# Kernel tuning notes

Hardware: AMD Instinct MI355X
Metric: run time of the kernel (lower is better)

The kernel has to match this reference:

```python
import jax, jax.numpy as jnp
import numpy as np

N_USERS = 50000
N_ITEMS = 50000
E = 400000
S = 128   # in_feats_s (memory / GRU hidden)
T = 64    # in_feats_t (time encoding dim)
ED = 64   # edge feature dim
M = 2 * S + T + ED  # in_feats_m = 384

_BASIS_FREQ = jnp.asarray(1.0 / 10 ** np.linspace(0, 9, T), dtype=jnp.float32)


def time_encode(ts):
    # cos(ts * freq + phase), phase == 0
    return jnp.cos(ts[:, None] * _BASIS_FREQ[None, :])


def mean_message(src_mem, dst_mem, ts, e, src, dst, n_dst):
    # mail per edge: [E, 2S + T + ED]
    mail = jnp.concatenate(
        [src_mem[src], dst_mem[dst], time_encode(ts), e], axis=1)
    s = jax.ops.segment_sum(mail, dst, num_segments=n_dst)
    cnt = jax.ops.segment_sum(jnp.ones_like(ts), dst, num_segments=n_dst)
    return s / jnp.maximum(cnt, 1.0)[:, None]


def gru_step(x, h, w_ih, w_hh, b_ih, b_hh):
    # single-step PyTorch GRU; gate order r, z, n
    gi = x @ w_ih.T + b_ih
    gh = h @ w_hh.T + b_hh
    ir, iz, i_n = jnp.split(gi, 3, axis=1)
    hr, hz, h_n = jnp.split(gh, 3, axis=1)
    r = jax.nn.sigmoid(ir + hr)
    z = jax.nn.sigmoid(iz + hz)
    n = jnp.tanh(i_n + r * h_n)
    return (1.0 - z) * n + z * h


def setup_inputs() -> dict:
    key = jax.random.key(0)
    ks = jax.random.split(key, 16)
    sc = 1.0 / np.sqrt(S)
    return {
        "si":   jax.random.normal(ks[0], (N_USERS, S), jnp.float32),
        "sj":   jax.random.normal(ks[1], (N_ITEMS, S), jnp.float32),
        "si_r": jax.random.normal(ks[2], (N_ITEMS, S), jnp.float32),
        "sj_r": jax.random.normal(ks[3], (N_USERS, S), jnp.float32),
        "t":    jax.random.uniform(ks[4], (E,), jnp.float32),
        "t_r":  jax.random.uniform(ks[5], (E,), jnp.float32),
        "e":    jax.random.normal(ks[6], (E, ED), jnp.float32),
        "e_r":  jax.random.normal(ks[7], (E, ED), jnp.float32),
        "w_ih": jax.random.normal(ks[8], (3 * S, M), jnp.float32) * sc,
        "w_hh": jax.random.normal(ks[9], (3 * S, S), jnp.float32) * sc,
        "b_ih": jax.random.normal(ks[10], (3 * S,), jnp.float32) * sc,
        "b_hh": jax.random.normal(ks[11], (3 * S,), jnp.float32) * sc,
        "src_g":  jax.random.randint(ks[12], (E,), 0, N_USERS, jnp.int32),
        "dst_g":  jax.random.randint(ks[13], (E,), 0, N_ITEMS, jnp.int32),
        "src_gr": jax.random.randint(ks[14], (E,), 0, N_ITEMS, jnp.int32),
        "dst_gr": jax.random.randint(ks[15], (E,), 0, N_USERS, jnp.int32),
    }


def reference(si, sj, si_r, sj_r, t, t_r, e, e_r,
              w_ih, w_hh, b_ih, b_hh,
              src_g, dst_g, src_gr, dst_gr):
    # g: user -> item; g_r: item -> user
    mj = mean_message(si, sj, t, e, src_g, dst_g, N_ITEMS)       # messages to items
    mi = mean_message(si_r, sj_r, t_r, e_r, src_gr, dst_gr, N_USERS)  # messages to users
    si_out = gru_step(mi, sj_r, w_ih, w_hh, b_ih, b_hh)  # user memory update
    sj_out = gru_step(mj, sj, w_ih, w_hh, b_ih, b_hh)    # item memory update
    return (si_out, sj_out)
```

## Files before the change

### kernel.cpp

```cpp
#include <hip/hip_runtime.h>
#include <math.h>

#define NUSERS 50000
#define NITEMS 50000
#define NTOT   100000
#define NNODE  50000
#define NCHUNK 196
#define MTILES 6250
#define KDIM   512
#define NWAVES 8192

typedef __attribute__((ext_vector_type(4))) float f32x4;
typedef __attribute__((ext_vector_type(8))) short short8;
typedef unsigned int u32;

#define AS1 __attribute__((address_space(1)))
#define AS3 __attribute__((address_space(3)))

static __device__ __forceinline__ unsigned short f2bf(float f) {
  unsigned int u = __float_as_uint(f);
  u += 0x7fffu + ((u >> 16) & 1u);
  return (unsigned short)(u >> 16);
}

static __device__ __forceinline__ u32 pack2(float x, float y) {
  return (u32)f2bf(x) | ((u32)f2bf(y) << 16);
}

static __device__ __forceinline__ void gload_lds16(const void* g, void* l) {
  __builtin_amdgcn_global_load_lds((const AS1 u32*)g, (AS3 u32*)l, 16, 0, 0);
}

__global__ void pack_w_kernel(const float* __restrict__ w_ih,
                              const float* __restrict__ w_hh,
                              const float* __restrict__ b_ih,
                              const float* __restrict__ b_hh,
                              unsigned short* __restrict__ Wb,
                              float* __restrict__ bb) {
  int idx = blockIdx.x * 256 + threadIdx.x;
  int j = idx & 7, l = (idx >> 3) & 63, ktt = idx >> 9;
  int kt = ktt & 15, tt = ktt >> 4;
  int g = tt * 16 + (l & 15);
  int k = kt * 32 + (l >> 4) * 8 + j;
  float v;
  if (g < 256)      v = (k < 384) ? w_ih[g * 384 + k] : w_hh[g * 128 + (k - 384)];
  else if (g < 384) v = (k < 384) ? w_ih[g * 384 + k] : 0.0f;
  else              v = (k < 384) ? 0.0f : w_hh[(g - 128) * 128 + (k - 384)];
  Wb[idx] = f2bf(v);
  if (idx < 512) {
    float b = (idx < 256) ? (b_ih[idx] + b_hh[idx])
            : (idx < 384) ? b_ih[idx]
                          : b_hh[idx - 128];
    bb[idx] = b;
  }
}

__global__ void cast_mem_kernel(const float* __restrict__ si,
                                const float* __restrict__ si_r,
                                unsigned short* __restrict__ si_b,
                                unsigned short* __restrict__ sir_b) {
  int i = blockIdx.x * 256 + threadIdx.x;
  const float* src; unsigned short* dst; int off;
  if (i < 800000) { src = si;   dst = si_b;  off = i; }
  else            { src = si_r; dst = sir_b; off = i - 800000; }
  const f32x4* p = (const f32x4*)(src + (size_t)off * 8);
  f32x4 a = p[0], b = p[1];
  short8 o;
  o[0] = f2bf(a[0]); o[1] = f2bf(a[1]); o[2] = f2bf(a[2]); o[3] = f2bf(a[3]);
  o[4] = f2bf(b[0]); o[5] = f2bf(b[1]); o[6] = f2bf(b[2]); o[7] = f2bf(b[3]);
  *(short8*)(dst + (size_t)off * 8) = o;
}

__global__ void hist_kernel(const int* __restrict__ dst_g,
                            const int* __restrict__ dst_gr,
                            int* __restrict__ deg_j, int* __restrict__ deg_i, int E) {
  int i = blockIdx.x * 256 + threadIdx.x;
  if (i < E) atomicAdd(&deg_j[dst_g[i]], 1);
  else if (i < 2 * E) atomicAdd(&deg_i[dst_gr[i - E]], 1);
}

__global__ void chunksum_kernel(const int* __restrict__ deg_j,
                                const int* __restrict__ deg_i,
                                int* __restrict__ csum) {
  int c = blockIdx.x;
  const int* deg = (c < NCHUNK) ? deg_j : deg_i;
  int cc = (c < NCHUNK) ? c : c - NCHUNK;
  int t = threadIdx.x;
  int idx = cc * 256 + t;
  int v = (idx < NNODE) ? deg[idx] : 0;
  for (int off = 32; off; off >>= 1) v += __shfl_down(v, off, 64);
  __shared__ int wsum[4];
  if ((t & 63) == 0) wsum[t >> 6] = v;
  __syncthreads();
  if (t == 0) csum[c] = wsum[0] + wsum[1] + wsum[2] + wsum[3];
}

__global__ void chunkscan_kernel(const int* __restrict__ csum, int* __restrict__ coff) {
  int d = blockIdx.x;
  const int* cs = csum + d * NCHUNK;
  int* co = coff + d * NCHUNK;
  int t = threadIdx.x, lane = t & 63, w = t >> 6;
  int v = (t < NCHUNK) ? cs[t] : 0;
  int x = v;
  for (int off = 1; off < 64; off <<= 1) {
    int y = __shfl_up(x, off, 64);
    if (lane >= off) x += y;
  }
  __shared__ int wt[4];
  if (lane == 63) wt[w] = x;
  __syncthreads();
  int add = 0;
  for (int k = 0; k < 4; ++k) if (k < w) add += wt[k];
  if (t < NCHUNK) co[t] = add + x - v;
}

__global__ void localscan_kernel(const int* __restrict__ deg_j,
                                 const int* __restrict__ deg_i,
                                 const int* __restrict__ coff,
                                 int* __restrict__ rs_j, int* __restrict__ cur_j,
                                 int* __restrict__ rs_i, int* __restrict__ cur_i) {
  int c = blockIdx.x;
  bool dj = c < NCHUNK;
  const int* deg = dj ? deg_j : deg_i;
  int cc = dj ? c : c - NCHUNK;
  int* rs = dj ? rs_j : rs_i;
  int* cur = dj ? cur_j : cur_i;
  int base = coff[c];
  int t = threadIdx.x, lane = t & 63, w = t >> 6;
  int idx = cc * 256 + t;
  int v = (idx < NNODE) ? deg[idx] : 0;
  int x = v;
  for (int off = 1; off < 64; off <<= 1) {
    int y = __shfl_up(x, off, 64);
    if (lane >= off) x += y;
  }
  __shared__ int wt[4];
  if (lane == 63) wt[w] = x;
  __syncthreads();
  int add = 0;
  for (int k = 0; k < 4; ++k) if (k < w) add += wt[k];
  int ex = base + add + x - v;
  if (idx < NNODE) { rs[idx] = ex; cur[idx] = ex; }
}

__global__ void fill_kernel(const int* __restrict__ src_g, const int* __restrict__ dst_g,
                            const float* __restrict__ t,
                            const int* __restrict__ src_gr, const int* __restrict__ dst_gr,
                            const float* __restrict__ t_r,
                            int* __restrict__ cur_j, int* __restrict__ cur_i,
                            int4* __restrict__ recP_j, int4* __restrict__ recP_i,
                            int E) {
  int i = blockIdx.x * 256 + threadIdx.x;
  if (i < E) {
    int pos = atomicAdd(&cur_j[dst_g[i]], 1);
    recP_j[pos] = make_int4(src_g[i], i, __float_as_int(t[i]), 0);
  } else if (i < 2 * E) {
    int k = i - E;
    int pos = atomicAdd(&cur_i[dst_gr[k]], 1);
    recP_i[pos] = make_int4(src_gr[k], k, __float_as_int(t_r[k]), 0);
  }
}

__global__ __launch_bounds__(256) void gather_kernel(
    const unsigned short* __restrict__ si_b, const unsigned short* __restrict__ sir_b,
    const float* __restrict__ sj, const float* __restrict__ sj_r,
    const float* __restrict__ e, const float* __restrict__ e_r,
    const int* __restrict__ rs_j, const int* __restrict__ rs_i,
    const int* __restrict__ deg_j, const int* __restrict__ deg_i,
    const int4* __restrict__ recP_j, const int4* __restrict__ recP_i,
    unsigned short* __restrict__ Xb) {
  __shared__ __align__(16) unsigned short rowbuf[4][512];
  int wid = threadIdx.x >> 6, lane = threadIdx.x & 63;
  int gwave = blockIdx.x * 4 + wid;
  float freq = __expf((float)lane * -0.3289407276f);
  unsigned short* rb = rowbuf[wid];
  u32* rb32 = (u32*)rb;

  for (int node = gwave; node < NTOT; node += NWAVES) {
    bool user = node < NUSERS;
    int idx = user ? node : node - NUSERS;
    const unsigned short* smem = user ? sir_b : si_b;
    const float* h  = user ? sj_r : sj;
    const float* ef = user ? e_r : e;
    int start = __builtin_amdgcn_readfirstlane((user ? rs_i : rs_j)[idx]);
    int deg   = __builtin_amdgcn_readfirstlane((user ? deg_i : deg_j)[idx]);
    const int4* rec = user ? recP_i : recP_j;

    float2 hvf = *(const float2*)(h + (size_t)idx * 128 + 2 * lane);

    float asx = 0.f, asy = 0.f;
    float at  = 0.f;
    float ae  = 0.f;

    for (int base = 0; base < deg; base += 64) {
      int nn = deg - base; if (nn > 64) nn = 64;
      int cl = (lane < nn) ? base + lane : base + nn - 1;
      int4 r = rec[start + cl];
      int full = nn & ~7;
      for (int j0 = 0; j0 < full; j0 += 8) {
        int s0 = __builtin_amdgcn_readlane(r.x, j0 + 0), e0 = __builtin_amdgcn_readlane(r.y, j0 + 0);
        int s1 = __builtin_amdgcn_readlane(r.x, j0 + 1), e1 = __builtin_amdgcn_readlane(r.y, j0 + 1);
        int s2 = __builtin_amdgcn_readlane(r.x, j0 + 2), e2 = __builtin_amdgcn_readlane(r.y, j0 + 2);
        int s3 = __builtin_amdgcn_readlane(r.x, j0 + 3), e3 = __builtin_amdgcn_readlane(r.y, j0 + 3);
        int s4 = __builtin_amdgcn_readlane(r.x, j0 + 4), e4 = __builtin_amdgcn_readlane(r.y, j0 + 4);
        int s5 = __builtin_amdgcn_readlane(r.x, j0 + 5), e5 = __builtin_amdgcn_readlane(r.y, j0 + 5);
        int s6 = __builtin_amdgcn_readlane(r.x, j0 + 6), e6 = __builtin_amdgcn_readlane(r.y, j0 + 6);
        int s7 = __builtin_amdgcn_readlane(r.x, j0 + 7), e7 = __builtin_amdgcn_readlane(r.y, j0 + 7);

        u32 v0 = *(const u32*)(smem + ((size_t)s0 << 7) + 2 * lane);
        u32 v1 = *(const u32*)(smem + ((size_t)s1 << 7) + 2 * lane);
        u32 v2 = *(const u32*)(smem + ((size_t)s2 << 7) + 2 * lane);
        u32 v3 = *(const u32*)(smem + ((size_t)s3 << 7) + 2 * lane);
        u32 v4 = *(const u32*)(smem + ((size_t)s4 << 7) + 2 * lane);
        u32 v5 = *(const u32*)(smem + ((size_t)s5 << 7) + 2 * lane);
        u32 v6 = *(const u32*)(smem + ((size_t)s6 << 7) + 2 * lane);
        u32 v7 = *(const u32*)(smem + ((size_t)s7 << 7) + 2 * lane);
        float f0 = ef[((size_t)e0 << 6) + lane];
        float f1 = ef[((size_t)e1 << 6) + lane];
        float f2 = ef[((size_t)e2 << 6) + lane];
        float f3 = ef[((size_t)e3 << 6) + lane];
        float f4 = ef[((size_t)e4 << 6) + lane];
        float f5 = ef[((size_t)e5 << 6) + lane];
        float f6 = ef[((size_t)e6 << 6) + lane];
        float f7 = ef[((size_t)e7 << 6) + lane];

        float c0 = __cosf(__int_as_float(__builtin_amdgcn_readlane(r.z, j0 + 0)) * freq);
        float c1 = __cosf(__int_as_float(__builtin_amdgcn_readlane(r.z, j0 + 1)) * freq);
        float c2 = __cosf(__int_as_float(__builtin_amdgcn_readlane(r.z, j0 + 2)) * freq);
        float c3 = __cosf(__int_as_float(__builtin_amdgcn_readlane(r.z, j0 + 3)) * freq);
        float c4 = __cosf(__int_as_float(__builtin_amdgcn_readlane(r.z, j0 + 4)) * freq);
        float c5 = __cosf(__int_as_float(__builtin_amdgcn_readlane(r.z, j0 + 5)) * freq);
        float c6 = __cosf(__int_as_float(__builtin_amdgcn_readlane(r.z, j0 + 6)) * freq);
        float c7 = __cosf(__int_as_float(__builtin_amdgcn_readlane(r.z, j0 + 7)) * freq);

        float l0 = __uint_as_float(v0 << 16), g0 = __uint_as_float(v0 & 0xffff0000u);
        float l1 = __uint_as_float(v1 << 16), g1 = __uint_as_float(v1 & 0xffff0000u);
        float l2 = __uint_as_float(v2 << 16), g2 = __uint_as_float(v2 & 0xffff0000u);
        float l3 = __uint_as_float(v3 << 16), g3 = __uint_as_float(v3 & 0xffff0000u);
        float l4 = __uint_as_float(v4 << 16), g4 = __uint_as_float(v4 & 0xffff0000u);
        float l5 = __uint_as_float(v5 << 16), g5 = __uint_as_float(v5 & 0xffff0000u);
        float l6 = __uint_as_float(v6 << 16), g6 = __uint_as_float(v6 & 0xffff0000u);
        float l7 = __uint_as_float(v7 << 16), g7 = __uint_as_float(v7 & 0xffff0000u);

        asx += ((l0 + l1) + (l2 + l3)) + ((l4 + l5) + (l6 + l7));
        asy += ((g0 + g1) + (g2 + g3)) + ((g4 + g5) + (g6 + g7));
        at  += ((c0 + c1) + (c2 + c3)) + ((c4 + c5) + (c6 + c7));
        ae  += ((f0 + f1) + (f2 + f3)) + ((f4 + f5) + (f6 + f7));
      }
      if (full < nn) {
        int j0 = full;
        int j1 = (j0 + 1 < nn) ? j0 + 1 : nn - 1;
        int j2 = (j0 + 2 < nn) ? j0 + 2 : nn - 1;
        int j3 = (j0 + 3 < nn) ? j0 + 3 : nn - 1;
        int j4 = (j0 + 4 < nn) ? j0 + 4 : nn - 1;
        int j5 = (j0 + 5 < nn) ? j0 + 5 : nn - 1;
        int j6 = (j0 + 6 < nn) ? j0 + 6 : nn - 1;
        float w1 = (j0 + 1 < nn) ? 1.0f : 0.0f;
        float w2 = (j0 + 2 < nn) ? 1.0f : 0.0f;
        float w3 = (j0 + 3 < nn) ? 1.0f : 0.0f;
        float w4 = (j0 + 4 < nn) ? 1.0f : 0.0f;
        float w5 = (j0 + 5 < nn) ? 1.0f : 0.0f;
        float w6 = (j0 + 6 < nn) ? 1.0f : 0.0f;

        int s0 = __builtin_amdgcn_readlane(r.x, j0), e0 = __builtin_amdgcn_readlane(r.y, j0);
        int s1 = __builtin_amdgcn_readlane(r.x, j1), e1 = __builtin_amdgcn_readlane(r.y, j1);
        int s2 = __builtin_amdgcn_readlane(r.x, j2), e2 = __builtin_amdgcn_readlane(r.y, j2);
        int s3 = __builtin_amdgcn_readlane(r.x, j3), e3 = __builtin_amdgcn_readlane(r.y, j3);
        int s4 = __builtin_amdgcn_readlane(r.x, j4), e4 = __builtin_amdgcn_readlane(r.y, j4);
        int s5 = __builtin_amdgcn_readlane(r.x, j5), e5 = __builtin_amdgcn_readlane(r.y, j5);
        int s6 = __builtin_amdgcn_readlane(r.x, j6), e6 = __builtin_amdgcn_readlane(r.y, j6);

        u32 v0 = *(const u32*)(smem + ((size_t)s0 << 7) + 2 * lane);
        u32 v1 = *(const u32*)(smem + ((size_t)s1 << 7) + 2 * lane);
        u32 v2 = *(const u32*)(smem + ((size_t)s2 << 7) + 2 * lane);
        u32 v3 = *(const u32*)(smem + ((size_t)s3 << 7) + 2 * lane);
        u32 v4 = *(const u32*)(smem + ((size_t)s4 << 7) + 2 * lane);
        u32 v5 = *(const u32*)(smem + ((size_t)s5 << 7) + 2 * lane);
        u32 v6 = *(const u32*)(smem + ((size_t)s6 << 7) + 2 * lane);
        float f0 = ef[((size_t)e0 << 6) + lane];
        float f1 = ef[((size_t)e1 << 6) + lane];
        float f2 = ef[((size_t)e2 << 6) + lane];
        float f3 = ef[((size_t)e3 << 6) + lane];
        float f4 = ef[((size_t)e4 << 6) + lane];
        float f5 = ef[((size_t)e5 << 6) + lane];
        float f6 = ef[((size_t)e6 << 6) + lane];

        float c0 = __cosf(__int_as_float(__builtin_amdgcn_readlane(r.z, j0)) * freq);
        float c1 = __cosf(__int_as_float(__builtin_amdgcn_readlane(r.z, j1)) * freq);
        float c2 = __cosf(__int_as_float(__builtin_amdgcn_readlane(r.z, j2)) * freq);
        float c3 = __cosf(__int_as_float(__builtin_amdgcn_readlane(r.z, j3)) * freq);
        float c4 = __cosf(__int_as_float(__builtin_amdgcn_readlane(r.z, j4)) * freq);
        float c5 = __cosf(__int_as_float(__builtin_amdgcn_readlane(r.z, j5)) * freq);
        float c6 = __cosf(__int_as_float(__builtin_amdgcn_readlane(r.z, j6)) * freq);

        float l0 = __uint_as_float(v0 << 16), g0 = __uint_as_float(v0 & 0xffff0000u);
        float l1 = __uint_as_float(v1 << 16), g1 = __uint_as_float(v1 & 0xffff0000u);
        float l2 = __uint_as_float(v2 << 16), g2 = __uint_as_float(v2 & 0xffff0000u);
        float l3 = __uint_as_float(v3 << 16), g3 = __uint_as_float(v3 & 0xffff0000u);
        float l4 = __uint_as_float(v4 << 16), g4 = __uint_as_float(v4 & 0xffff0000u);
        float l5 = __uint_as_float(v5 << 16), g5 = __uint_as_float(v5 & 0xffff0000u);
        float l6 = __uint_as_float(v6 << 16), g6 = __uint_as_float(v6 & 0xffff0000u);

        asx += l0 + w1 * l1 + w2 * l2 + w3 * l3 + w4 * l4 + w5 * l5 + w6 * l6;
        asy += g0 + w1 * g1 + w2 * g2 + w3 * g3 + w4 * g4 + w5 * g5 + w6 * g6;
        at  += c0 + w1 * c1 + w2 * c2 + w3 * c3 + w4 * c4 + w5 * c5 + w6 * c6;
        ae  += f0 + w1 * f1 + w2 * f2 + w3 * f3 + w4 * f4 + w5 * f5 + w6 * f6;
      }
    }

    float invc = (deg > 0) ? 1.0f / (float)deg : 0.0f;
    float hz   = (deg > 0) ? 1.0f : 0.0f;

    rb32[lane]       = pack2(asx * invc, asy * invc);
    rb32[64 + lane]  = pack2(hvf.x * hz, hvf.y * hz);
    rb[256 + lane]   = f2bf(at * invc);
    rb[320 + lane]   = f2bf(ae * invc);
    rb32[192 + lane] = pack2(hvf.x, hvf.y);

    short8 vv = *(const short8*)(rb + lane * 8);
    *(short8*)(Xb + (size_t)node * 512 + lane * 8) = vv;
  }
}

__global__ __launch_bounds__(1024, 4) void gemm_gru_kernel(
    const unsigned short* __restrict__ Xb,
    const unsigned short* __restrict__ Wb,
    const float* __restrict__ bb,
    const float* __restrict__ sj_r,
    const float* __restrict__ sj,
    float* __restrict__ out) {
  __shared__ __align__(16) unsigned short sA[32768];
  __shared__ __align__(16) unsigned short sW[2][16384];
  int wid = threadIdx.x >> 6, lane = threadIdx.x & 63;
  int mg = wid >> 3, cg = wid & 7;
  int mbase = blockIdx.x * 4;
  int col16 = lane & 15, quad = lane >> 4;

  f32x4 acc[2][4];
#pragma unroll
  for (int mi = 0; mi < 2; ++mi)
#pragma unroll
    for (int g = 0; g < 4; ++g) acc[mi][g] = (f32x4)0.0f;

#pragma unroll
  for (int i = 0; i < 4; ++i) {
    int u = wid * 4 + i;
    int mt = mbase + (u >> 4);
    if (mt >= MTILES) mt = MTILES - 1;
    const unsigned short* gp = Xb + (size_t)(mt * 16 + (lane & 15)) * 512
                                  + (u & 15) * 32 + (lane >> 4) * 8;
    gload_lds16(gp, sA + u * 512);
  }
#pragma unroll
  for (int i = 0; i < 2; ++i) {
    int tt = wid * 2 + i;
    const unsigned short* gp = Wb + ((size_t)(tt * 16 + 0) * 64 + lane) * 8;
    gload_lds16(gp, sW[0] + tt * 512);
  }
  __syncthreads();

  const unsigned short* aBase = sA + (size_t)(mg * 32) * 512 + lane * 8;

  for (int kt = 0; kt < 16; ++kt) {
    int cur = kt & 1;
    if (kt < 15) {
#pragma unroll
      for (int i = 0; i < 2; ++i) {
        int tt = wid * 2 + i;
        const unsigned short* gp = Wb + ((size_t)(tt * 16 + kt + 1) * 64 + lane) * 8;
        gload_lds16(gp, sW[cur ^ 1] + tt * 512);
      }
    }
    short8 a0 = *(const short8*)(aBase + (size_t)kt * 512);
    short8 a1 = *(const short8*)(aBase + (size_t)(16 + kt) * 512);
    short8 b0 = *(const short8*)(sW[cur] + (0 * 8 + cg) * 512 + lane * 8);
    short8 b1 = *(const short8*)(sW[cur] + (1 * 8 + cg) * 512 + lane * 8);
    short8 b2 = *(const short8*)(sW[cur] + (2 * 8 + cg) * 512 + lane * 8);
    short8 b3 = *(const short8*)(sW[cur] + (3 * 8 + cg) * 512 + lane * 8);
    acc[0][0] = __builtin_amdgcn_mfma_f32_16x16x32_bf16(a0, b0, acc[0][0], 0, 0, 0);
    acc[0][1] = __builtin_amdgcn_mfma_f32_16x16x32_bf16(a0, b1, acc[0][1], 0, 0, 0);
    acc[0][2] = __builtin_amdgcn_mfma_f32_16x16x32_bf16(a0, b2, acc[0][2], 0, 0, 0);
    acc[0][3] = __builtin_amdgcn_mfma_f32_16x16x32_bf16(a0, b3, acc[0][3], 0, 0, 0);
    acc[1][0] = __builtin_amdgcn_mfma_f32_16x16x32_bf16(a1, b0, acc[1][0], 0, 0, 0);
    acc[1][1] = __builtin_amdgcn_mfma_f32_16x16x32_bf16(a1, b1, acc[1][1], 0, 0, 0);
    acc[1][2] = __builtin_amdgcn_mfma_f32_16x16x32_bf16(a1, b2, acc[1][2], 0, 0, 0);
    acc[1][3] = __builtin_amdgcn_mfma_f32_16x16x32_bf16(a1, b3, acc[1][3], 0, 0, 0);
    __syncthreads();
  }

  int cc = cg * 16 + col16;
  float bbr = bb[cc], bbz = bb[128 + cc], bbn = bb[256 + cc], bbh = bb[384 + cc];
#pragma unroll
  for (int mi = 0; mi < 2; ++mi) {
    int mt = mbase + mg * 2 + mi;
    if (mt >= MTILES) continue;
#pragma unroll
    for (int r = 0; r < 4; ++r) {
      int row = mt * 16 + quad * 4 + r;
      float rp  = acc[mi][0][r] + bbr;
      float zp  = acc[mi][1][r] + bbz;
      float inp = acc[mi][2][r] + bbn;
      float hnp = acc[mi][3][r] + bbh;
      float rg = 1.0f / (1.0f + __expf(-rp));
      float zg = 1.0f / (1.0f + __expf(-zp));
      float ng = tanhf(inp + rg * hnp);
      float hv = (row < NUSERS) ? sj_r[(size_t)row * 128 + cc]
                                : sj[(size_t)(row - NUSERS) * 128 + cc];
      out[(size_t)row * 128 + cc] = (1.0f - zg) * ng + zg * hv;
    }
  }
}

extern "C" void kernel_launch(void* const* d_in, const int* in_sizes, int n_in,
                              void* d_out, int out_size, void* d_ws, size_t ws_size,
                              hipStream_t stream) {
  const float* si   = (const float*)d_in[0];
  const float* sj   = (const float*)d_in[1];
  const float* si_r = (const float*)d_in[2];
  const float* sj_r = (const float*)d_in[3];
  const float* t    = (const float*)d_in[4];
  const float* t_r  = (const float*)d_in[5];
  const float* e    = (const float*)d_in[6];
  const float* e_r  = (const float*)d_in[7];
  const float* w_ih = (const float*)d_in[8];
  const float* w_hh = (const float*)d_in[9];
  const float* b_ih = (const float*)d_in[10];
  const float* b_hh = (const float*)d_in[11];
  const int* src_g  = (const int*)d_in[12];
  const int* dst_g  = (const int*)d_in[13];
  const int* src_gr = (const int*)d_in[14];
  const int* dst_gr = (const int*)d_in[15];
  int E = in_sizes[4];

  unsigned short* Xb = (unsigned short*)d_ws;
  unsigned short* Wb = Xb + (size_t)NTOT * 512;
  float* bb   = (float*)(Wb + 262144);
  int* deg_j  = (int*)(bb + 512);
  int* deg_i  = deg_j + NNODE;
  int* rs_j   = deg_i + NNODE;
  int* rs_i   = rs_j + NNODE;
  int* cur_j  = rs_i + NNODE;
  int* cur_i  = cur_j + NNODE;
  int* csum   = cur_i + NNODE;
  int* coff   = csum + 2 * NCHUNK;
  int4* recP_j = (int4*)(coff + 2 * NCHUNK);
  int4* recP_i = recP_j + E;
  unsigned short* si_b  = (unsigned short*)(recP_i + E);
  unsigned short* sir_b = si_b + 6400000;

  hipMemsetAsync(deg_j, 0, 2 * NNODE * sizeof(int), stream);

  pack_w_kernel<<<(512 * 512) / 256, 256, 0, stream>>>(w_ih, w_hh, b_ih, b_hh, Wb, bb);
  cast_mem_kernel<<<6250, 256, 0, stream>>>(si, si_r, si_b, sir_b);

  int blks2E = (2 * E + 255) / 256;
  hist_kernel<<<blks2E, 256, 0, stream>>>(dst_g, dst_gr, deg_j, deg_i, E);
  chunksum_kernel<<<2 * NCHUNK, 256, 0, stream>>>(deg_j, deg_i, csum);
  chunkscan_kernel<<<2, 256, 0, stream>>>(csum, coff);
  localscan_kernel<<<2 * NCHUNK, 256, 0, stream>>>(deg_j, deg_i, coff, rs_j, cur_j, rs_i, cur_i);
  fill_kernel<<<blks2E, 256, 0, stream>>>(src_g, dst_g, t, src_gr, dst_gr, t_r,
                                          cur_j, cur_i, recP_j, recP_i, E);

  gather_kernel<<<NWAVES / 4, 256, 0, stream>>>(si_b, sir_b, sj, sj_r, e, e_r,
                                                rs_j, rs_i, deg_j, deg_i,
                                                recP_j, recP_i, Xb);

  float* out = (float*)d_out;
  gemm_gru_kernel<<<(MTILES + 3) / 4, 1024, 0, stream>>>(Xb, Wb, bb, sj_r, sj, out);
}
```

Measured before the change: 592.5 us.

## Keep weight slice resident in LDS and stream A tiles from global

The GEMM+GRU kernel is restructured so each block loads a fixed quarter of the packed weight matrix (two 16-column groups across all four gates, full K) into LDS once. Each wave then reads its four 16-row A tiles straight from global memory and accumulates a 4x8 MFMA tile. This drops the per-k-step weight double-buffering and barriers. In exchange, every A row is read from global by four different blocks, so A traffic through L2 rises. Register pressure also grows from 32 accumulators per wave, and the weight slice uses 128KB of LDS per block.

```diff
diff --git a/kernel.cpp b/kernel.cpp
--- a/kernel.cpp
+++ b/kernel.cpp
@@ -7,6 +7,7 @@
 #define NNODE  50000
 #define NCHUNK 196
 #define MTILES 6250
+#define NMCHUNK 196
 #define KDIM   512
 #define NWAVES 8192
 
@@ -322,91 +323,81 @@
   }
 }
 
-__global__ __launch_bounds__(1024, 4) void gemm_gru_kernel(
+__global__ __launch_bounds__(512, 2) void gemm_gru_kernel(
     const unsigned short* __restrict__ Xb,
     const unsigned short* __restrict__ Wb,
     const float* __restrict__ bb,
     const float* __restrict__ sj_r,
     const float* __restrict__ sj,
     float* __restrict__ out) {
-  __shared__ __align__(16) unsigned short sA[32768];
-  __shared__ __align__(16) unsigned short sW[2][16384];
+  __shared__ __align__(16) unsigned short sW[65536];
   int wid = threadIdx.x >> 6, lane = threadIdx.x & 63;
-  int mg = wid >> 3, cg = wid & 7;
-  int mbase = blockIdx.x * 4;
+  int jp = blockIdx.x & 3;
+  int mcbase = (blockIdx.x >> 2) * 32;
   int col16 = lane & 15, quad = lane >> 4;
 
-  f32x4 acc[2][4];
-#pragma unroll
-  for (int mi = 0; mi < 2; ++mi)
-#pragma unroll
-    for (int g = 0; g < 4; ++g) acc[mi][g] = (f32x4)0.0f;
-
-#pragma unroll
-  for (int i = 0; i < 4; ++i) {
-    int u = wid * 4 + i;
-    int mt = mbase + (u >> 4);
-    if (mt >= MTILES) mt = MTILES - 1;
-    const unsigned short* gp = Xb + (size_t)(mt * 16 + (lane & 15)) * 512
-                                  + (u & 15) * 32 + (lane >> 4) * 8;
-    gload_lds16(gp, sA + u * 512);
-  }
-#pragma unroll
-  for (int i = 0; i < 2; ++i) {
-    int tt = wid * 2 + i;
-    const unsigned short* gp = Wb + ((size_t)(tt * 16 + 0) * 64 + lane) * 8;
-    gload_lds16(gp, sW[0] + tt * 512);
+  {
+    int g = wid >> 1, p = wid & 1;
+    int tt = g * 8 + jp * 2 + p;
+    const unsigned short* wp = Wb + ((size_t)tt * 16 * 64 + lane) * 8;
+#pragma unroll
+    for (int kt = 0; kt < 16; ++kt)
+      gload_lds16(wp + (size_t)kt * 512, sW + (wid * 16 + kt) * 512);
   }
   __syncthreads();
 
-  const unsigned short* aBase = sA + (size_t)(mg * 32) * 512 + lane * 8;
+  int mt[4];
+  const unsigned short* Ap[4];
+#pragma unroll
+  for (int mi = 0; mi < 4; ++mi) {
+    mt[mi] = mcbase + wid * 4 + mi;
+    int mc = (mt[mi] < MTILES) ? mt[mi] : MTILES - 1;
+    Ap[mi] = Xb + (size_t)(mc * 16 + col16) * 512 + quad * 8;
+  }
+
+  f32x4 acc[4][8];
+#pragma unroll
+  for (int mi = 0; mi < 4; ++mi)
+#pragma unroll
+    for (int t8 = 0; t8 < 8; ++t8) acc[mi][t8] = (f32x4)0.0f;
 
   for (int kt = 0; kt < 16; ++kt) {
-    int cur = kt & 1;
-    if (kt < 15) {
-#pragma unroll
-      for (int i = 0; i < 2; ++i) {
-        int tt = wid * 2 + i;
-        const unsigned short* gp = Wb + ((size_t)(tt * 16 + kt + 1) * 64 + lane) * 8;
-        gload_lds16(gp, sW[cur ^ 1] + tt * 512);
+    short8 a[4];
+#pragma unroll
+    for (int mi = 0; mi < 4; ++mi)
+      a[mi] = *(const short8*)(Ap[mi] + kt * 32);
+    short8 b[8];
+#pragma unroll
+    for (int t8 = 0; t8 < 8; ++t8)
+      b[t8] = *(const short8*)(sW + (t8 * 16 + kt) * 512 + lane * 8);
+#pragma unroll
+    for (int mi = 0; mi < 4; ++mi)
+#pragma unroll
+      for (int t8 = 0; t8 < 8; ++t8)
+        acc[mi][t8] = __builtin_amdgcn_mfma_f32_16x16x32_bf16(a[mi], b[t8], acc[mi][t8], 0, 0, 0);
+  }
+
+#pragma unroll
+  for (int p = 0; p < 2; ++p) {
+    int cc = (jp * 2 + p) * 16 + col16;
+    float bbr = bb[cc], bbz = bb[128 + cc], bbn = bb[256 + cc], bbh = bb[384 + cc];
+#pragma unroll
+    for (int mi = 0; mi < 4; ++mi) {
+      if (mt[mi] >= MTILES) continue;
+#pragma unroll
+      for (int r = 0; r < 4; ++r) {
+        int row = mt[mi] * 16 + quad * 4 + r;
+        float rp  = acc[mi][0 + p][r] + bbr;
+        float zp  = acc[mi][2 + p][r] + bbz;
+        float inp = acc[mi][4 + p][r] + bbn;
+        float hnp = acc[mi][6 + p][r] + bbh;
+        float rg = 1.0f / (1.0f + __expf(-rp));
+        float zg = 1.0f / (1.0f + __expf(-zp));
+        float ng = tanhf(inp + rg * hnp);
+        float hv = (row < NUSERS) ? sj_r[(size_t)row * 128 + cc]
+                                  : sj[(size_t)(row - NUSERS) * 128 + cc];
+        out[(size_t)row * 128 + cc] = (1.0f - zg) * ng + zg * hv;
       }
-    }
-    short8 a0 = *(const short8*)(aBase + (size_t)kt * 512);
-    short8 a1 = *(const short8*)(aBase + (size_t)(16 + kt) * 512);
-    short8 b0 = *(const short8*)(sW[cur] + (0 * 8 + cg) * 512 + lane * 8);
-    short8 b1 = *(const short8*)(sW[cur] + (1 * 8 + cg) * 512 + lane * 8);
-    short8 b2 = *(const short8*)(sW[cur] + (2 * 8 + cg) * 512 + lane * 8);
-    short8 b3 = *(const short8*)(sW[cur] + (3 * 8 + cg) * 512 + lane * 8);
-    acc[0][0] = __builtin_amdgcn_mfma_f32_16x16x32_bf16(a0, b0, acc[0][0], 0, 0, 0);
-    acc[0][1] = __builtin_amdgcn_mfma_f32_16x16x32_bf16(a0, b1, acc[0][1], 0, 0, 0);
-    acc[0][2] = __builtin_amdgcn_mfma_f32_16x16x32_bf16(a0, b2, acc[0][2], 0, 0, 0);
-    acc[0][3] = __builtin_amdgcn_mfma_f32_16x16x32_bf16(a0, b3, acc[0][3], 0, 0, 0);
-    acc[1][0] = __builtin_amdgcn_mfma_f32_16x16x32_bf16(a1, b0, acc[1][0], 0, 0, 0);
-    acc[1][1] = __builtin_amdgcn_mfma_f32_16x16x32_bf16(a1, b1, acc[1][1], 0, 0, 0);
-    acc[1][2] = __builtin_amdgcn_mfma_f32_16x16x32_bf16(a1, b2, acc[1][2], 0, 0, 0);
-    acc[1][3] = __builtin_amdgcn_mfma_f32_16x16x32_bf16(a1, b3, acc[1][3], 0, 0, 0);
-    __syncthreads();
-  }
-
-  int cc = cg * 16 + col16;
-  float bbr = bb[cc], bbz = bb[128 + cc], bbn = bb[256 + cc], bbh = bb[384 + cc];
-#pragma unroll
-  for (int mi = 0; mi < 2; ++mi) {
-    int mt = mbase + mg * 2 + mi;
-    if (mt >= MTILES) continue;
-#pragma unroll
-    for (int r = 0; r < 4; ++r) {
-      int row = mt * 16 + quad * 4 + r;
-      float rp  = acc[mi][0][r] + bbr;
-      float zp  = acc[mi][1][r] + bbz;
-      float inp = acc[mi][2][r] + bbn;
-      float hnp = acc[mi][3][r] + bbh;
-      float rg = 1.0f / (1.0f + __expf(-rp));
-      float zg = 1.0f / (1.0f + __expf(-zp));
-      float ng = tanhf(inp + rg * hnp);
-      float hv = (row < NUSERS) ? sj_r[(size_t)row * 128 + cc]
-                                : sj[(size_t)(row - NUSERS) * 128 + cc];
-      out[(size_t)row * 128 + cc] = (1.0f - zg) * ng + zg * hv;
     }
   }
 }
@@ -466,5 +457,5 @@
                                                 recP_j, recP_i, Xb);
 
   float* out = (float*)d_out;
-  gemm_gru_kernel<<<(MTILES + 3) / 4, 1024, 0, stream>>>(Xb, Wb, bb, sj_r, sj, out);
-}
+  gemm_gru_kernel<<<NMCHUNK * 4, 512, 0, stream>>>(Xb, Wb, bb, sj_r, sj, out);
+}
```

Measured after the change: 622.9 us. 1.05x slower.
